# Kernel optimization log

Measured on AMD Instinct MI355X. Metric: run time of the kernel, lower is better.

Reference implementation:

```python
import jax, jax.numpy as jnp
import numpy as np

B, S, H = 1, 2048, 1024
E, INTER, TOP_K = 8, 2048, 2
ALPHA, LIMIT = 1.702, 7.0


def setup_inputs() -> dict:
    key = jax.random.key(0)
    ks = jax.random.split(key, 7)
    sc = 0.02
    return {
        'hidden_states': jax.random.normal(ks[0], (B, S, H), jnp.float32),
        'router_w': jax.random.normal(ks[1], (H, E), jnp.float32) * sc,
        'router_b': jax.random.normal(ks[2], (E,), jnp.float32) * sc,
        'gate_up_proj': jax.random.normal(ks[3], (E, H, 2 * INTER), jnp.float32) * sc,
        'gate_up_bias': jax.random.normal(ks[4], (E, 2 * INTER), jnp.float32) * sc,
        'down_proj': jax.random.normal(ks[5], (E, INTER, H), jnp.float32) * sc,
        'down_bias': jax.random.normal(ks[6], (E, H), jnp.float32) * sc,
    }


def reference(hidden_states, router_w, router_b, gate_up_proj, gate_up_bias, down_proj, down_bias):
    x = hidden_states  # [B,S,H]
    # router: top-k over expert logits, softmax over selected logits (gpt-oss style)
    logits = jnp.einsum('bsh,he->bse', x, router_w) + router_b
    top_vals, top_idx = jax.lax.top_k(logits, TOP_K)          # [B,S,K]
    topk_weights = jax.nn.softmax(top_vals, axis=-1)          # [B,S,K]
    # dense per-expert gate_up GEMM (dispatch is identity on 1 device)
    gu = jnp.einsum('bsh,ehn->besn', x, gate_up_proj)         # [B,E,S,2I]
    gu = gu + gate_up_bias[None, :, None, :]
    gate = jnp.minimum(gu[..., :INTER], LIMIT)
    up = jnp.clip(gu[..., INTER:], -LIMIT, LIMIT)
    glu = gate * jax.nn.sigmoid(gate * ALPHA)
    act = (up + 1.0) * glu                                    # [B,E,S,I]
    down = jnp.einsum('besl,elh->besh', act, down_proj)       # [B,E,S,H]
    down = down + down_bias[None, :, None, :]
    # combine: gather each token's K selected expert outputs, weight and sum
    down_bseh = jnp.transpose(down, (0, 2, 1, 3))             # [B,S,E,H]
    idx = jnp.broadcast_to(top_idx[..., None], (B, S, TOP_K, H))
    sel = jnp.take_along_axis(down_bseh, idx, axis=2)         # [B,S,K,H]
    return (sel * topk_weights[..., None]).sum(axis=2)        # [B,S,H]
```

## Files before the change

### kernel.cpp

```cpp
#include <hip/hip_runtime.h>
#include <hip/hip_bf16.h>
#include <math.h>

#define S 2048
#define H 1024
#define NE 8
#define INTER 2048
#define ALPHA 1.702f
#define LIMIT 7.0f

typedef __bf16 bf16x8 __attribute__((ext_vector_type(8)));
typedef float f32x4 __attribute__((ext_vector_type(4)));

#define WS_COUNTS 0
#define WS_SLOTS  4096
#define WS_W      (WS_SLOTS + NE*S*4)
#define WS_XB     (WS_W + 2*S*4)
#define WS_GUP    (WS_XB + (size_t)S*H*2)
#define WS_DPN    (WS_GUP + (size_t)NE*2*INTER*H*2)
#define WS_ACT    (WS_DPN + (size_t)NE*H*INTER*2)

static __device__ __forceinline__ unsigned short f2bf(float f) {
    union { __hip_bfloat16 h; unsigned short u; } cv;
    cv.h = __float2bfloat16(f);
    return cv.u;
}

static __device__ __forceinline__ void gload16(const void* g, void* l) {
    __builtin_amdgcn_global_load_lds(
        (const __attribute__((address_space(1))) unsigned int*)(unsigned long long)g,
        (__attribute__((address_space(3))) unsigned int*)(unsigned int)(unsigned long long)l,
        16, 0, 0);
}

__global__ __launch_bounds__(64) void router_kernel(
    const float* __restrict__ x, const float* __restrict__ rw,
    const float* __restrict__ rb, int* __restrict__ counts,
    int* __restrict__ slots, float* __restrict__ slot_w)
{
    int tok = blockIdx.x;
    int lane = threadIdx.x;
    float acc[NE];
#pragma unroll
    for (int e = 0; e < NE; ++e) acc[e] = 0.f;
    const float* xr = x + (size_t)tok * H;
    for (int h = lane; h < H; h += 64) {
        float xv = xr[h];
        const float* wr = rw + (size_t)h * NE;
#pragma unroll
        for (int e = 0; e < NE; ++e) acc[e] += xv * wr[e];
    }
#pragma unroll
    for (int e = 0; e < NE; ++e) {
#pragma unroll
        for (int off = 32; off > 0; off >>= 1)
            acc[e] += __shfl_down(acc[e], off);
    }
    if (lane == 0) {
        float v[NE];
#pragma unroll
        for (int e = 0; e < NE; ++e) v[e] = acc[e] + rb[e];
        int i1 = 0; float v1 = v[0];
#pragma unroll
        for (int e = 1; e < NE; ++e) if (v[e] > v1) { v1 = v[e]; i1 = e; }
        int i2 = -1; float v2 = -3.0e38f;
#pragma unroll
        for (int e = 0; e < NE; ++e) if (e != i1 && v[e] > v2) { v2 = v[e]; i2 = e; }
        float w1 = 1.f / (1.f + expf(v2 - v1));
        float w2 = 1.f - w1;
        int p1 = atomicAdd(&counts[i1], 1);
        slots[i1 * S + p1] = tok * 2;
        slot_w[tok * 2] = w1;
        int p2 = atomicAdd(&counts[i2], 1);
        slots[i2 * S + p2] = tok * 2 + 1;
        slot_w[tok * 2 + 1] = w2;
    }
}

__global__ __launch_bounds__(256) void conv_x(const float* __restrict__ in,
                                              unsigned short* __restrict__ out)
{
    int i = blockIdx.x * 256 + threadIdx.x;
    float4 v = ((const float4*)in)[i];
    ushort4 o;
    o.x = f2bf(v.x); o.y = f2bf(v.y); o.z = f2bf(v.z); o.w = f2bf(v.w);
    ((ushort4*)out)[i] = o;
}

__global__ __launch_bounds__(256) void transpose_bf16(
    const float* __restrict__ in, unsigned short* __restrict__ out,
    int K, int N, int in_stride, int in_coloff,
    size_t in_zstride, size_t out_zstride)
{
    __shared__ float tile[32][33];
    const float* ip = in + blockIdx.z * in_zstride;
    unsigned short* op = out + blockIdx.z * out_zstride;
    int k0 = blockIdx.x * 32, n0 = blockIdx.y * 32;
    int t = threadIdx.x;
    int lk = t >> 3, ln = (t & 7) * 4;
    float4 v = *(const float4*)(ip + (size_t)(k0 + lk) * in_stride + in_coloff + n0 + ln);
    tile[lk][ln + 0] = v.x; tile[lk][ln + 1] = v.y;
    tile[lk][ln + 2] = v.z; tile[lk][ln + 3] = v.w;
    __syncthreads();
    int on = t >> 3, ok = (t & 7) * 4;
    ushort4 o;
    o.x = f2bf(tile[ok + 0][on]); o.y = f2bf(tile[ok + 1][on]);
    o.z = f2bf(tile[ok + 2][on]); o.w = f2bf(tile[ok + 3][on]);
    *(ushort4*)(op + (size_t)(n0 + on) * K + k0 + ok) = o;
}

__global__ __launch_bounds__(256) void gateup_mfma(
    const unsigned short* __restrict__ xb,
    const unsigned short* __restrict__ gw,
    const float* __restrict__ gub,
    const int* __restrict__ counts, const int* __restrict__ slots,
    unsigned short* __restrict__ act)
{
    int e = blockIdx.z;
    int cnt = counts[e];
    int m0 = blockIdx.y * 128;
    if (m0 >= cnt) return;
    int n0 = blockIdx.x * 64;

    __shared__ unsigned short As[128 * 32];
    __shared__ unsigned short Gs[64 * 32];
    __shared__ unsigned short Us[64 * 32];
    __shared__ int sl[128];

    int t = threadIdx.x;
    int lane = t & 63, w = t >> 6;
    if (t < 128) {
        int r = m0 + t;
        sl[t] = slots[e * S + (r < cnt ? r : cnt - 1)];
    }
    __syncthreads();

    int quad = lane >> 4, l16 = lane & 15;
    int wm = (w >> 1) * 64, wn = (w & 1) * 32;

    int ar0 = w * 32 + (lane >> 2);
    int ar1 = ar0 + 16;
    const unsigned short* ap0 = xb + (size_t)(sl[ar0] >> 1) * H + (lane & 3) * 8;
    const unsigned short* ap1 = xb + (size_t)(sl[ar1] >> 1) * H + (lane & 3) * 8;
    int bn = w * 16 + (lane >> 2);
    const unsigned short* gp = gw + (size_t)e * 2 * INTER * H + (size_t)(n0 + bn) * H + (lane & 3) * 8;
    const unsigned short* up = gp + (size_t)INTER * H;

    unsigned short* la0 = &As[(2 * w) * 512 + lane * 8];
    unsigned short* la1 = &As[(2 * w + 1) * 512 + lane * 8];
    unsigned short* lg = &Gs[w * 512 + lane * 8];
    unsigned short* lu = &Us[w * 512 + lane * 8];

    f32x4 accg[4][2], accu[4][2];
#pragma unroll
    for (int mi = 0; mi < 4; ++mi)
#pragma unroll
        for (int ni = 0; ni < 2; ++ni) {
            accg[mi][ni] = (f32x4){0.f, 0.f, 0.f, 0.f};
            accu[mi][ni] = (f32x4){0.f, 0.f, 0.f, 0.f};
        }

    for (int k0 = 0; k0 < H; k0 += 32) {
        __syncthreads();
        gload16(ap0 + k0, la0);
        gload16(ap1 + k0, la1);
        gload16(gp + k0, lg);
        gload16(up + k0, lu);
        __syncthreads();
        bf16x8 af[4], gf[2], uf[2];
#pragma unroll
        for (int mi = 0; mi < 4; ++mi)
            af[mi] = *(const bf16x8*)&As[(wm + mi * 16 + l16) * 32 + quad * 8];
#pragma unroll
        for (int ni = 0; ni < 2; ++ni) {
            gf[ni] = *(const bf16x8*)&Gs[(wn + ni * 16 + l16) * 32 + quad * 8];
            uf[ni] = *(const bf16x8*)&Us[(wn + ni * 16 + l16) * 32 + quad * 8];
        }
#pragma unroll
        for (int mi = 0; mi < 4; ++mi)
#pragma unroll
            for (int ni = 0; ni < 2; ++ni) {
                accg[mi][ni] = __builtin_amdgcn_mfma_f32_16x16x32_bf16(af[mi], gf[ni], accg[mi][ni], 0, 0, 0);
                accu[mi][ni] = __builtin_amdgcn_mfma_f32_16x16x32_bf16(af[mi], uf[ni], accu[mi][ni], 0, 0, 0);
            }
    }

    const float* gb = gub + (size_t)e * 2 * INTER;
#pragma unroll
    for (int mi = 0; mi < 4; ++mi) {
#pragma unroll
        for (int r = 0; r < 4; ++r) {
            int rt = wm + mi * 16 + quad * 4 + r;
            if (m0 + rt >= cnt) continue;
            int slot = sl[rt];
            unsigned short* orow = act + (size_t)slot * INTER;
#pragma unroll
            for (int ni = 0; ni < 2; ++ni) {
                int col = n0 + wn + ni * 16 + l16;
                float gate = accg[mi][ni][r] + gb[col];
                float uv = accu[mi][ni][r] + gb[INTER + col];
                gate = fminf(gate, LIMIT);
                uv = fminf(fmaxf(uv, -LIMIT), LIMIT);
                float glu = gate / (1.f + __expf(-ALPHA * gate));
                orow[col] = f2bf((uv + 1.f) * glu);
            }
        }
    }
}

__global__ __launch_bounds__(256) void down_mfma(
    const unsigned short* __restrict__ act,
    const unsigned short* __restrict__ dw,
    const float* __restrict__ db,
    const int* __restrict__ counts, const int* __restrict__ slots,
    const float* __restrict__ slot_w,
    float* __restrict__ out)
{
    int e = blockIdx.z;
    int cnt = counts[e];
    int m0 = blockIdx.y * 128;
    if (m0 >= cnt) return;
    int n0 = blockIdx.x * 64;

    __shared__ unsigned short As[128 * 32];
    __shared__ unsigned short Bs[64 * 32];
    __shared__ int sl[128];

    int t = threadIdx.x;
    int lane = t & 63, w = t >> 6;
    if (t < 128) {
        int r = m0 + t;
        sl[t] = slots[e * S + (r < cnt ? r : cnt - 1)];
    }
    __syncthreads();

    int quad = lane >> 4, l16 = lane & 15;
    int wm = (w >> 1) * 64, wn = (w & 1) * 32;

    int ar0 = w * 32 + (lane >> 2);
    int ar1 = ar0 + 16;
    const unsigned short* ap0 = act + (size_t)sl[ar0] * INTER + (lane & 3) * 8;
    const unsigned short* ap1 = act + (size_t)sl[ar1] * INTER + (lane & 3) * 8;
    int bn = w * 16 + (lane >> 2);
    const unsigned short* bp = dw + (size_t)e * H * INTER + (size_t)(n0 + bn) * INTER + (lane & 3) * 8;

    unsigned short* la0 = &As[(2 * w) * 512 + lane * 8];
    unsigned short* la1 = &As[(2 * w + 1) * 512 + lane * 8];
    unsigned short* lb = &Bs[w * 512 + lane * 8];

    f32x4 acc[4][2];
#pragma unroll
    for (int mi = 0; mi < 4; ++mi)
#pragma unroll
        for (int ni = 0; ni < 2; ++ni)
            acc[mi][ni] = (f32x4){0.f, 0.f, 0.f, 0.f};

    for (int k0 = 0; k0 < INTER; k0 += 32) {
        __syncthreads();
        gload16(ap0 + k0, la0);
        gload16(ap1 + k0, la1);
        gload16(bp + k0, lb);
        __syncthreads();
        bf16x8 af[4], bf[2];
#pragma unroll
        for (int mi = 0; mi < 4; ++mi)
            af[mi] = *(const bf16x8*)&As[(wm + mi * 16 + l16) * 32 + quad * 8];
#pragma unroll
        for (int ni = 0; ni < 2; ++ni)
            bf[ni] = *(const bf16x8*)&Bs[(wn + ni * 16 + l16) * 32 + quad * 8];
#pragma unroll
        for (int mi = 0; mi < 4; ++mi)
#pragma unroll
            for (int ni = 0; ni < 2; ++ni)
                acc[mi][ni] = __builtin_amdgcn_mfma_f32_16x16x32_bf16(af[mi], bf[ni], acc[mi][ni], 0, 0, 0);
    }

    const float* dbr = db + (size_t)e * H;
#pragma unroll
    for (int mi = 0; mi < 4; ++mi) {
#pragma unroll
        for (int r = 0; r < 4; ++r) {
            int rt = wm + mi * 16 + quad * 4 + r;
            if (m0 + rt >= cnt) continue;
            int slot = sl[rt];
            int tok = slot >> 1;
            float wgt = slot_w[slot];
#pragma unroll
            for (int ni = 0; ni < 2; ++ni) {
                int col = n0 + wn + ni * 16 + l16;
                float rr = acc[mi][ni][r] + dbr[col];
                atomicAdd(&out[(size_t)tok * H + col], wgt * rr);
            }
        }
    }
}

extern "C" void kernel_launch(void* const* d_in, const int* in_sizes, int n_in,
                              void* d_out, int out_size, void* d_ws, size_t ws_size,
                              hipStream_t stream)
{
    const float* x   = (const float*)d_in[0];
    const float* rw  = (const float*)d_in[1];
    const float* rb  = (const float*)d_in[2];
    const float* gup = (const float*)d_in[3];
    const float* gub = (const float*)d_in[4];
    const float* dp  = (const float*)d_in[5];
    const float* db  = (const float*)d_in[6];
    float* out = (float*)d_out;

    char* ws = (char*)d_ws;
    int* counts            = (int*)(ws + WS_COUNTS);
    int* slots             = (int*)(ws + WS_SLOTS);
    float* slot_w          = (float*)(ws + WS_W);
    unsigned short* xb     = (unsigned short*)(ws + WS_XB);
    unsigned short* gw     = (unsigned short*)(ws + WS_GUP);
    unsigned short* dw     = (unsigned short*)(ws + WS_DPN);
    unsigned short* act    = (unsigned short*)(ws + WS_ACT);

    hipMemsetAsync(counts, 0, 4096, stream);
    hipMemsetAsync(out, 0, (size_t)S * H * sizeof(float), stream);

    conv_x<<<(S * H) / (256 * 4), 256, 0, stream>>>(x, xb);
    transpose_bf16<<<dim3(H / 32, INTER / 32, NE), 256, 0, stream>>>(
        gup, gw, H, INTER, 2 * INTER, 0,
        (size_t)H * 2 * INTER, (size_t)2 * INTER * H);
    transpose_bf16<<<dim3(H / 32, INTER / 32, NE), 256, 0, stream>>>(
        gup, gw + (size_t)INTER * H, H, INTER, 2 * INTER, INTER,
        (size_t)H * 2 * INTER, (size_t)2 * INTER * H);
    transpose_bf16<<<dim3(INTER / 32, H / 32, NE), 256, 0, stream>>>(
        dp, dw, INTER, H, H, 0,
        (size_t)INTER * H, (size_t)H * INTER);

    router_kernel<<<S, 64, 0, stream>>>(x, rw, rb, counts, slots, slot_w);

    gateup_mfma<<<dim3(INTER / 64, 16, NE), 256, 0, stream>>>(
        xb, gw, gub, counts, slots, act);

    down_mfma<<<dim3(H / 64, 16, NE), 256, 0, stream>>>(
        act, dw, db, counts, slots, slot_w, out);
}
```

Before: 481.2 us.

## Fuse router with x conversion, merge weight transposes, split-K down GEMM

The router kernel now also converts x to bf16 while it reads each row, which removes the separate conv_x launch and a second pass over x. The three weight transpose launches are merged into one prep kernel that uses 64x64 tiles, converts to bf16 before storing to LDS, and writes 16-byte vectors. The down GEMM is split along K into two halves, doubling the grid so more blocks can run. The cost is twice as many atomic adds to the output, with the bias added only by the first half.

```diff
diff --git a/kernel.cpp b/kernel.cpp
--- a/kernel.cpp
+++ b/kernel.cpp
@@ -11,6 +11,7 @@
 
 typedef __bf16 bf16x8 __attribute__((ext_vector_type(8)));
 typedef float f32x4 __attribute__((ext_vector_type(4)));
+typedef unsigned short u16x8 __attribute__((ext_vector_type(8)));
 
 #define WS_COUNTS 0
 #define WS_SLOTS  4096
@@ -33,22 +34,30 @@
         16, 0, 0);
 }
 
-__global__ __launch_bounds__(64) void router_kernel(
+__global__ __launch_bounds__(64) void router_conv(
     const float* __restrict__ x, const float* __restrict__ rw,
     const float* __restrict__ rb, int* __restrict__ counts,
-    int* __restrict__ slots, float* __restrict__ slot_w)
+    int* __restrict__ slots, float* __restrict__ slot_w,
+    unsigned short* __restrict__ xb)
 {
     int tok = blockIdx.x;
     int lane = threadIdx.x;
+    const float4* xr = (const float4*)(x + (size_t)tok * H);
+    ushort4* xo = (ushort4*)(xb + (size_t)tok * H);
     float acc[NE];
 #pragma unroll
     for (int e = 0; e < NE; ++e) acc[e] = 0.f;
-    const float* xr = x + (size_t)tok * H;
-    for (int h = lane; h < H; h += 64) {
-        float xv = xr[h];
-        const float* wr = rw + (size_t)h * NE;
-#pragma unroll
-        for (int e = 0; e < NE; ++e) acc[e] += xv * wr[e];
+#pragma unroll
+    for (int p = 0; p < H / 256; ++p) {
+        int idx = p * 64 + lane;
+        float4 v = xr[idx];
+        ushort4 o;
+        o.x = f2bf(v.x); o.y = f2bf(v.y); o.z = f2bf(v.z); o.w = f2bf(v.w);
+        xo[idx] = o;
+        const float* wr = rw + (size_t)idx * 4 * NE;
+#pragma unroll
+        for (int e = 0; e < NE; ++e)
+            acc[e] += v.x * wr[e] + v.y * wr[NE + e] + v.z * wr[2 * NE + e] + v.w * wr[3 * NE + e];
     }
 #pragma unroll
     for (int e = 0; e < NE; ++e) {
@@ -77,36 +86,53 @@
     }
 }
 
-__global__ __launch_bounds__(256) void conv_x(const float* __restrict__ in,
-                                              unsigned short* __restrict__ out)
-{
-    int i = blockIdx.x * 256 + threadIdx.x;
-    float4 v = ((const float4*)in)[i];
-    ushort4 o;
-    o.x = f2bf(v.x); o.y = f2bf(v.y); o.z = f2bf(v.z); o.w = f2bf(v.w);
-    ((ushort4*)out)[i] = o;
-}
-
-__global__ __launch_bounds__(256) void transpose_bf16(
-    const float* __restrict__ in, unsigned short* __restrict__ out,
-    int K, int N, int in_stride, int in_coloff,
-    size_t in_zstride, size_t out_zstride)
-{
-    __shared__ float tile[32][33];
-    const float* ip = in + blockIdx.z * in_zstride;
-    unsigned short* op = out + blockIdx.z * out_zstride;
-    int k0 = blockIdx.x * 32, n0 = blockIdx.y * 32;
+__global__ __launch_bounds__(256) void prep(
+    const float* __restrict__ gup, const float* __restrict__ dp,
+    unsigned short* __restrict__ gw, unsigned short* __restrict__ dw)
+{
+    int z = blockIdx.y;
+    int e = z / 3, which = z % 3;
+    const float* in;
+    unsigned short* out;
+    int K, N, istride;
+    if (which == 0) {
+        in = gup + (size_t)e * H * 2 * INTER;
+        out = gw + (size_t)e * 2 * INTER * H;
+        K = H; N = INTER; istride = 2 * INTER;
+    } else if (which == 1) {
+        in = gup + (size_t)e * H * 2 * INTER + INTER;
+        out = gw + (size_t)e * 2 * INTER * H + (size_t)INTER * H;
+        K = H; N = INTER; istride = 2 * INTER;
+    } else {
+        in = dp + (size_t)e * INTER * H;
+        out = dw + (size_t)e * H * INTER;
+        K = INTER; N = H; istride = H;
+    }
+    int ntiles = N / 64;
+    int k0 = (blockIdx.x / ntiles) * 64;
+    int n0 = (blockIdx.x % ntiles) * 64;
+
+    __shared__ unsigned short tile[64][68];
     int t = threadIdx.x;
-    int lk = t >> 3, ln = (t & 7) * 4;
-    float4 v = *(const float4*)(ip + (size_t)(k0 + lk) * in_stride + in_coloff + n0 + ln);
-    tile[lk][ln + 0] = v.x; tile[lk][ln + 1] = v.y;
-    tile[lk][ln + 2] = v.z; tile[lk][ln + 3] = v.w;
+    int lk = t >> 4, ln = (t & 15) * 4;
+#pragma unroll
+    for (int p = 0; p < 4; ++p) {
+        int kk = lk + p * 16;
+        float4 v = *(const float4*)(in + (size_t)(k0 + kk) * istride + n0 + ln);
+        ushort4 o;
+        o.x = f2bf(v.x); o.y = f2bf(v.y); o.z = f2bf(v.z); o.w = f2bf(v.w);
+        *(ushort4*)&tile[kk][ln] = o;
+    }
     __syncthreads();
-    int on = t >> 3, ok = (t & 7) * 4;
-    ushort4 o;
-    o.x = f2bf(tile[ok + 0][on]); o.y = f2bf(tile[ok + 1][on]);
-    o.z = f2bf(tile[ok + 2][on]); o.w = f2bf(tile[ok + 3][on]);
-    *(ushort4*)(op + (size_t)(n0 + on) * K + k0 + ok) = o;
+    int wn = t >> 3, wk = (t & 7) * 8;
+#pragma unroll
+    for (int p = 0; p < 2; ++p) {
+        int nn = wn + p * 32;
+        u16x8 o;
+#pragma unroll
+        for (int i = 0; i < 8; ++i) o[i] = tile[wk + i][nn];
+        *(u16x8*)(out + (size_t)(n0 + nn) * K + k0 + wk) = o;
+    }
 }
 
 __global__ __launch_bounds__(256) void gateup_mfma(
@@ -216,7 +242,8 @@
     const float* __restrict__ slot_w,
     float* __restrict__ out)
 {
-    int e = blockIdx.z;
+    int e = blockIdx.z >> 1;
+    int ks = blockIdx.z & 1;
     int cnt = counts[e];
     int m0 = blockIdx.y * 128;
     if (m0 >= cnt) return;
@@ -239,10 +266,11 @@
 
     int ar0 = w * 32 + (lane >> 2);
     int ar1 = ar0 + 16;
-    const unsigned short* ap0 = act + (size_t)sl[ar0] * INTER + (lane & 3) * 8;
-    const unsigned short* ap1 = act + (size_t)sl[ar1] * INTER + (lane & 3) * 8;
+    int kbase = ks * (INTER / 2);
+    const unsigned short* ap0 = act + (size_t)sl[ar0] * INTER + kbase + (lane & 3) * 8;
+    const unsigned short* ap1 = act + (size_t)sl[ar1] * INTER + kbase + (lane & 3) * 8;
     int bn = w * 16 + (lane >> 2);
-    const unsigned short* bp = dw + (size_t)e * H * INTER + (size_t)(n0 + bn) * INTER + (lane & 3) * 8;
+    const unsigned short* bp = dw + (size_t)e * H * INTER + (size_t)(n0 + bn) * INTER + kbase + (lane & 3) * 8;
 
     unsigned short* la0 = &As[(2 * w) * 512 + lane * 8];
     unsigned short* la1 = &As[(2 * w + 1) * 512 + lane * 8];
@@ -255,7 +283,7 @@
         for (int ni = 0; ni < 2; ++ni)
             acc[mi][ni] = (f32x4){0.f, 0.f, 0.f, 0.f};
 
-    for (int k0 = 0; k0 < INTER; k0 += 32) {
+    for (int k0 = 0; k0 < INTER / 2; k0 += 32) {
         __syncthreads();
         gload16(ap0 + k0, la0);
         gload16(ap1 + k0, la1);
@@ -288,7 +316,7 @@
 #pragma unroll
             for (int ni = 0; ni < 2; ++ni) {
                 int col = n0 + wn + ni * 16 + l16;
-                float rr = acc[mi][ni][r] + dbr[col];
+                float rr = acc[mi][ni][r] + (ks == 0 ? dbr[col] : 0.f);
                 atomicAdd(&out[(size_t)tok * H + col], wgt * rr);
             }
         }
@@ -320,22 +348,13 @@
     hipMemsetAsync(counts, 0, 4096, stream);
     hipMemsetAsync(out, 0, (size_t)S * H * sizeof(float), stream);
 
-    conv_x<<<(S * H) / (256 * 4), 256, 0, stream>>>(x, xb);
-    transpose_bf16<<<dim3(H / 32, INTER / 32, NE), 256, 0, stream>>>(
-        gup, gw, H, INTER, 2 * INTER, 0,
-        (size_t)H * 2 * INTER, (size_t)2 * INTER * H);
-    transpose_bf16<<<dim3(H / 32, INTER / 32, NE), 256, 0, stream>>>(
-        gup, gw + (size_t)INTER * H, H, INTER, 2 * INTER, INTER,
-        (size_t)H * 2 * INTER, (size_t)2 * INTER * H);
-    transpose_bf16<<<dim3(INTER / 32, H / 32, NE), 256, 0, stream>>>(
-        dp, dw, INTER, H, H, 0,
-        (size_t)INTER * H, (size_t)H * INTER);
-
-    router_kernel<<<S, 64, 0, stream>>>(x, rw, rb, counts, slots, slot_w);
+    router_conv<<<S, 64, 0, stream>>>(x, rw, rb, counts, slots, slot_w, xb);
+
+    prep<<<dim3(512, NE * 3), 256, 0, stream>>>(gup, dp, gw, dw);
 
     gateup_mfma<<<dim3(INTER / 64, 16, NE), 256, 0, stream>>>(
         xb, gw, gub, counts, slots, act);
 
-    down_mfma<<<dim3(H / 64, 16, NE), 256, 0, stream>>>(
+    down_mfma<<<dim3(H / 64, 16, NE * 2), 256, 0, stream>>>(
         act, dw, db, counts, slots, slot_w, out);
 }
```

New measurement: 450.7 us. 6.3% less time.
